# Kernel tuning notes

Hardware: AMD Instinct MI355X
Metric: run time of the kernel (lower is better)

## Reference

```python
import jax, jax.numpy as jnp
import numpy as np

T, B, E, H = 512, 64, 256, 256


def setup_inputs() -> dict:
    key = jax.random.key(0)
    ks = jax.random.split(key, 9)
    x = jax.random.normal(ks[0], (T * B, E), dtype=jnp.float32)
    # packed-sequence time reversal for equal-length sequences
    t = jnp.arange(T * B, dtype=jnp.int32)
    ix_mapping = (T - 1 - t // B) * B + (t % B)
    s = 0.05
    fw_W0 = jax.random.normal(ks[1], (3, E + H, H), dtype=jnp.float32) * s
    fw_W1 = jax.random.normal(ks[2], (3, 2 * H + H, H), dtype=jnp.float32) * s
    bw_W0 = jax.random.normal(ks[3], (3, E + H, H), dtype=jnp.float32) * s
    bw_W1 = jax.random.normal(ks[4], (3, 2 * H + H, H), dtype=jnp.float32) * s
    fw_b0 = jnp.zeros((3, H), jnp.float32)
    fw_b1 = jnp.zeros((3, H), jnp.float32)
    bw_b0 = jnp.zeros((3, H), jnp.float32)
    bw_b1 = jnp.zeros((3, H), jnp.float32)
    return dict(x=x, ix_mapping=ix_mapping, fw_W0=fw_W0, fw_b0=fw_b0,
                fw_W1=fw_W1, fw_b1=fw_b1, bw_W0=bw_W0, bw_b0=bw_b0,
                bw_W1=bw_W1, bw_b1=bw_b1)


def _run_direction(X_packed, W, b):
    # X_packed: [T*B, Din]; W: [3, Din+H, H] (r, h, z gates); b: [3, H]
    Din = X_packed.shape[1]
    X = X_packed.reshape(T, B, Din)

    def step(h, x_t):
        xh = jnp.concatenate((x_t, h), axis=1)          # [B, Din+H]
        r = jax.nn.sigmoid(xh @ W[0] + b[0])
        z = jax.nn.sigmoid(xh @ W[2] + b[2])
        xhr = jnp.concatenate((x_t, r * h), axis=1)
        cand = jnp.tanh(xhr @ W[1] + b[1])
        h_new = z * h + (1.0 - z) * cand
        return h_new, h_new

    h0 = jnp.zeros((B, X_packed.shape[1] * 0 + W.shape[2]), X_packed.dtype)
    h_n, states = jax.lax.scan(step, h0, X)
    return states.reshape(T * B, -1), h_n


def reference(x, ix_mapping, fw_W0, fw_b0, fw_W1, fw_b1,
              bw_W0, bw_b0, bw_W1, bw_b1):
    fwd_in = x
    bwd_in = x[ix_mapping]
    fw_params = [(fw_W0, fw_b0), (fw_W1, fw_b1)]
    bw_params = [(bw_W0, bw_b0), (bw_W1, bw_b1)]
    n_layers = len(fw_params)
    fh, bh = [], []
    for layer in range(n_layers):
        fs, fhn = _run_direction(fwd_in, *fw_params[layer])
        bs, bhn = _run_direction(bwd_in, *bw_params[layer])
        fh.append(fhn)
        bh.append(bhn)
        if layer < n_layers - 1:
            fwd_in = jnp.concatenate((fs, bs[ix_mapping]), axis=1)
            bwd_in = jnp.concatenate((bs, fs[ix_mapping]), axis=1)
    # MergeMethod.CONCAT
    out = jnp.concatenate((fs, bs[ix_mapping]), axis=1)  # [T*B, 2H]
    return out, jnp.stack(fh), jnp.stack(bh)
```

## Files before the change

kernel.cpp:

```cpp
#include <hip/hip_runtime.h>
#include <hip/hip_bf16.h>

#define T_STEPS 512
#define BATCH 64
#define TB (T_STEPS * BATCH)

typedef short bf16x8 __attribute__((ext_vector_type(8)));
typedef float f32x4 __attribute__((ext_vector_type(4)));

union FragU { uint4 u; bf16x8 v; };

static __device__ __forceinline__ bf16x8 ld_frag(const uint4* p) {
  FragU f; f.u = *p; return f.v;
}

static __device__ __forceinline__ unsigned short f2bf(float f) {
  unsigned u = __float_as_uint(f);
  return (unsigned short)((u + 0x7FFFu + ((u >> 16) & 1u)) >> 16);
}

static __device__ __forceinline__ unsigned cvt_pk_bf16(float lo, float hi) {
  unsigned r;
  asm("v_cvt_pk_bf16_f32 %0, %1, %2" : "=v"(r) : "v"(lo), "v"(hi));
  return r;
}

static __device__ __forceinline__ int revrow(int r) {
  int t = r >> 6, b = r & 63;
  return ((T_STEPS - 1 - t) << 6) | b;
}

#define S_RZ  (-1.4426950408889634f)
#define S_C   (-2.8853900817779268f)

#define AWR(N, x) asm volatile("v_accvgpr_write_b32 a" #N ", %0" :: "v"(x) : "a" #N)
#define LOADF(F, A0, A1, A2, A3) do { \
    const int c_ = (F) >> 3, kt_ = (F) & 7; \
    const int nt_ = (c_ < 2) ? (w * 2 + c_) : (14 + w * 2 + c_); \
    uint4 t = whrzp[((size_t)nt_ * 8 + kt_) * 64 + lane]; \
    AWR(A0, t.x); AWR(A1, t.y); AWR(A2, t.z); AWR(A3, t.w); } while (0)

#define MFMA_A(acc, va, B0, B3) \
  asm volatile("v_mfma_f32_16x16x32_bf16 %0, %1, a[" #B0 ":" #B3 "], %0" \
               : "+v"(acc) : "v"(va))
#define MFMA_A1(acc, va, B0, B3) \
  asm volatile("s_nop 1\n\tv_mfma_f32_16x16x32_bf16 %0, %1, a[" #B0 ":" #B3 "], %0" \
               : "+v"(acc) : "v"(va))
#define MFMA_V(acc, va, vb) \
  asm volatile("v_mfma_f32_16x16x32_bf16 %0, %1, %2, %0" \
               : "+v"(acc) : "v"(va), "v"(vb))
#define MFMA_V1(acc, va, vb) \
  asm volatile("s_nop 1\n\tv_mfma_f32_16x16x32_bf16 %0, %1, %2, %0" \
               : "+v"(acc) : "v"(va), "v"(vb))
#define ACCFENCE2(a, b) asm volatile("s_nop 7\n\ts_nop 7" : "+v"(a), "+v"(b))
#define ACCFENCE4(a, b, c, d) \
  asm volatile("s_nop 7\n\ts_nop 7" : "+v"(a), "+v"(b), "+v"(c), "+v"(d))

#define ACLB \
  "a0","a1","a2","a3","a4","a5","a6","a7","a8","a9","a10","a11","a12","a13","a14","a15", \
  "a16","a17","a18","a19","a20","a21","a22","a23","a24","a25","a26","a27","a28","a29","a30","a31", \
  "a32","a33","a34","a35","a36","a37","a38","a39","a40","a41","a42","a43","a44","a45","a46","a47", \
  "a48","a49","a50","a51","a52","a53","a54","a55","a56","a57","a58","a59","a60","a61","a62","a63", \
  "a64","a65","a66","a67","a68","a69","a70","a71","a72","a73","a74","a75","a76","a77","a78","a79", \
  "a80","a81","a82","a83","a84","a85","a86","a87","a88","a89","a90","a91","a92","a93","a94","a95", \
  "a96","a97","a98","a99","a100","a101","a102","a103","a104","a105","a106","a107","a108","a109","a110","a111", \
  "a112","a113","a114","a115","a116","a117","a118","a119","a120","a121","a122","a123","a124","a125","a126","a127"

__global__ void pack_w_kernel(const float* __restrict__ W, int rows, int k_base,
                              int n_tiles, int k_tiles, int mode,
                              unsigned short* __restrict__ dst) {
  int gid = blockIdx.x * blockDim.x + threadIdx.x;
  int total = n_tiles * k_tiles * 64;
  if (gid >= total) return;
  int lane = gid & 63;
  int fi = gid >> 6;
  int kt = fi % k_tiles;
  int nt = fi / k_tiles;
  int n = nt * 16 + (lane & 15);
  int g, col; float s;
  if (mode == 0)      { g = n >> 8;            col = n & 255; s = (g == 1) ? S_C : S_RZ; }
  else if (mode == 1) { g = (n < 256) ? 0 : 2; col = n & 255; s = S_RZ; }
  else                { g = 1;                 col = n;       s = S_C; }
  int k0 = k_base + kt * 32 + ((lane >> 4) << 3);
  const float* src = W + ((size_t)g * rows + k0) * 256 + col;
  unsigned short v[8];
#pragma unroll
  for (int j = 0; j < 8; ++j) v[j] = f2bf(src[(size_t)j * 256] * s);
  uint4 o;
  o.x = v[0] | ((unsigned)v[1] << 16);
  o.y = v[2] | ((unsigned)v[3] << 16);
  o.z = v[4] | ((unsigned)v[5] << 16);
  o.w = v[6] | ((unsigned)v[7] << 16);
  ((uint4*)dst)[gid] = o;
}

static __device__ __forceinline__ bf16x8 cvt8(float4 f0, float4 f1) {
  uint4 o;
  o.x = f2bf(f0.x) | ((unsigned)f2bf(f0.y) << 16);
  o.y = f2bf(f0.z) | ((unsigned)f2bf(f0.w) << 16);
  o.z = f2bf(f1.x) | ((unsigned)f2bf(f1.y) << 16);
  o.w = f2bf(f1.z) | ((unsigned)f2bf(f1.w) << 16);
  FragU f; f.u = o; return f.v;
}

template<int LAYER>
__global__ __launch_bounds__(256)
void gemm_xg_kernel(const float* __restrict__ x,
                    const unsigned short* __restrict__ fs0,
                    const unsigned short* __restrict__ bs0,
                    const unsigned short* __restrict__ Bp,
                    const float* __restrict__ bias_fw,
                    const float* __restrict__ bias_bw,
                    f32x4* __restrict__ Xg, int t0, int chunkT)
{
  constexpr int KT = (LAYER == 0) ? 8 : 16;
  int dir = blockIdx.z;
  int lane = threadIdx.x & 63;
  int w = threadIdx.x >> 6;
  int ww = w >> 1, wc = w & 1;
  int mt0 = blockIdx.x * 8 + ww * 4;
  int nt0 = blockIdx.y * 8 + wc * 4;
  const uint4* B = (const uint4*)Bp + (size_t)dir * 48 * KT * 64;
  const int arow = lane & 15;
  const int k0b = ((lane >> 4) << 3);

  f32x4 acc[4][4] = {};
#pragma unroll
  for (int kt = 0; kt < KT; ++kt) {
    int k0 = kt * 32 + k0b;
    bf16x8 a[4], b[4];
#pragma unroll
    for (int i = 0; i < 4; ++i) {
      int grow = t0 * 64 + (mt0 + i) * 16 + arow;
      if (LAYER == 0) {
        int gr = dir ? revrow(grow) : grow;
        const float4* s = (const float4*)(x + (size_t)gr * 256 + k0);
        a[i] = cvt8(s[0], s[1]);
      } else {
        const unsigned short* base; int r2 = grow, kk = k0;
        if (k0 < 256) { base = dir ? bs0 : fs0; }
        else          { base = dir ? fs0 : bs0; r2 = revrow(grow); kk = k0 - 256; }
        a[i] = *(const bf16x8*)(base + (size_t)r2 * 256 + kk);
      }
    }
#pragma unroll
    for (int j = 0; j < 4; ++j) b[j] = ld_frag(B + ((size_t)(nt0 + j) * KT + kt) * 64 + lane);
#pragma unroll
    for (int i = 0; i < 4; ++i)
#pragma unroll
      for (int j = 0; j < 4; ++j)
        acc[i][j] = __builtin_amdgcn_mfma_f32_16x16x32_bf16(a[i], b[j], acc[i][j], 0, 0, 0);
  }

  const float* bias = dir ? bias_bw : bias_fw;
  f32x4* C = Xg + (size_t)dir * (chunkT * 4) * 48 * 64;
#pragma unroll
  for (int j = 0; j < 4; ++j) {
    int ct = nt0 + j;
    int col = ct * 16 + (lane & 15);
    int g = col >> 8, cc = col & 255;
    float bv = ((g == 1) ? S_C : S_RZ) * bias[g * 256 + cc];
#pragma unroll
    for (int i = 0; i < 4; ++i) {
      int rt = blockIdx.x * 8 + ww * 4 + i;
      f32x4 v = acc[i][j];
      v[0] += bv; v[1] += bv; v[2] += bv; v[3] += bv;
      C[((size_t)rt * 48 + ct) * 64 + lane] = v;
    }
  }
}

template<int LAYER>
__global__ __launch_bounds__(512) __attribute__((amdgpu_waves_per_eu(2, 2)))
void gru_kernel(const f32x4* __restrict__ Xg,
                const uint4* __restrict__ whrz_fw, const uint4* __restrict__ whrz_bw,
                const uint4* __restrict__ whc_fw,  const uint4* __restrict__ whc_bw,
                unsigned short* __restrict__ sfw_bf, unsigned short* __restrict__ sbw_bf,
                float* __restrict__ out,
                float* __restrict__ hstate, float* __restrict__ dout_h,
                int t0, int chunkT)
{
  const int dir = blockIdx.y;
  const int bx = blockIdx.x;
  const int row0 = bx * 16;
  const int tid = threadIdx.x;
  const int lane = tid & 63;
  const int w = tid >> 6;

  __shared__ __align__(16) unsigned short h_bf[16 * 256];
  __shared__ __align__(16) unsigned short rh_bf[16 * 256];
  __shared__ __align__(16) uint4 wc_lds[16 * 8 * 64];

  const uint4* whrzp = dir ? whrz_bw : whrz_fw;
  const uint4* whcp  = dir ? whc_bw  : whc_fw;

  for (int i = tid; i < 16 * 8 * 64; i += 512) wc_lds[i] = whcp[i];

  LOADF(0, 0, 1, 2, 3);     LOADF(1, 4, 5, 6, 7);     LOADF(2, 8, 9, 10, 11);   LOADF(3, 12, 13, 14, 15);
  LOADF(4, 16, 17, 18, 19); LOADF(5, 20, 21, 22, 23); LOADF(6, 24, 25, 26, 27); LOADF(7, 28, 29, 30, 31);
  LOADF(8, 32, 33, 34, 35); LOADF(9, 36, 37, 38, 39); LOADF(10, 40, 41, 42, 43); LOADF(11, 44, 45, 46, 47);
  LOADF(12, 48, 49, 50, 51); LOADF(13, 52, 53, 54, 55); LOADF(14, 56, 57, 58, 59); LOADF(15, 60, 61, 62, 63);
  LOADF(16, 64, 65, 66, 67); LOADF(17, 68, 69, 70, 71); LOADF(18, 72, 73, 74, 75); LOADF(19, 76, 77, 78, 79);
  LOADF(20, 80, 81, 82, 83); LOADF(21, 84, 85, 86, 87); LOADF(22, 88, 89, 90, 91); LOADF(23, 92, 93, 94, 95);
  LOADF(24, 96, 97, 98, 99); LOADF(25, 100, 101, 102, 103); LOADF(26, 104, 105, 106, 107); LOADF(27, 108, 109, 110, 111);
  LOADF(28, 112, 113, 114, 115); LOADF(29, 116, 117, 118, 119); LOADF(30, 120, 121, 122, 123); LOADF(31, 124, 125, 126, 127);

  const int ccol = lane & 15;
  const int crow = ((lane >> 4) << 2);

  float* hst = hstate + (size_t)(dir * 4 + bx) * 4096;
  for (int i = tid; i < 16 * 256; i += 512) {
    float v = (t0 == 0) ? 0.0f : hst[i];
    int rr = i >> 8, cc = i & 255;
    int cb = cc * 2;
    int byt = rr * 512 + (((cb & ~15) ^ ((rr & 7) << 4)) | (cb & 15));
    *(unsigned short*)((char*)h_bf + byt) = f2bf(v);
  }
  float hreg[2][4];
#pragma unroll
  for (int j = 0; j < 2; ++j)
#pragma unroll
    for (int r = 0; r < 4; ++r) {
      int rr = crow + r, c = (w * 2 + j) * 16 + ccol;
      hreg[j][r] = (t0 == 0) ? 0.0f : hst[rr * 256 + c];
    }
  __syncthreads();

  const int ctR0 = w * 2, ctR1 = w * 2 + 1;
  const int ctZ0 = 32 + w * 2, ctZ1 = 33 + w * 2;
  const int ctB0c = 16 + w * 2, ctB1c = 17 + w * 2;
  const f32x4* XgD = Xg + (size_t)dir * (chunkT * 4) * 48 * 64;
  unsigned short* sp_bf = dir ? sbw_bf : sfw_bf;
  const int coff = dir ? 256 : 0;
  const int ardbase = (lane & 15) * 512;
  const int arxor = ((lane & 7) << 4);
  const int afc = ((lane >> 4) << 4);

#define AFRAG(KT) (*(const bf16x8*)((const char*)h_bf + (ardbase + ((KT * 64 + afc) ^ arxor))))
#define RFRAG(KT) (*(const bf16x8*)((const char*)rh_bf + (ardbase + ((KT * 64 + afc) ^ arxor))))
#define SWZ(rr, cb) ((rr) * 512 + ((((cb) & ~15) ^ (((rr) & 7) << 4)) | ((cb) & 15)))

  f32x4 xa0, xa1, xa2, xa3, xb0, xb1;
  {
    size_t rtb0 = ((size_t)(0 * 4 + bx) * 48) * 64 + lane;
    xa0 = XgD[rtb0 + (size_t)ctR0 * 64];
    xa1 = XgD[rtb0 + (size_t)ctR1 * 64];
    xa2 = XgD[rtb0 + (size_t)ctZ0 * 64];
    xa3 = XgD[rtb0 + (size_t)ctZ1 * 64];
    xb0 = XgD[rtb0 + (size_t)ctB0c * 64];
    xb1 = XgD[rtb0 + (size_t)ctB1c * 64];
  }

#pragma unroll 1
  for (int t = t0; t < t0 + chunkT; ++t) {
    const int tloc = t - t0;

    f32x4 accA0 = {}, accA1 = {}, accA2 = {}, accA3 = {};
    {
      bf16x8 af;
      af = AFRAG(0);
      MFMA_A1(accA0, af, 0, 3);   MFMA_A1(accA1, af, 32, 35);
      MFMA_A1(accA2, af, 64, 67); MFMA_A1(accA3, af, 96, 99);
      af = AFRAG(1);
      MFMA_A(accA0, af, 4, 7);    MFMA_A(accA1, af, 36, 39);
      MFMA_A(accA2, af, 68, 71);  MFMA_A(accA3, af, 100, 103);
      af = AFRAG(2);
      MFMA_A(accA0, af, 8, 11);   MFMA_A(accA1, af, 40, 43);
      MFMA_A(accA2, af, 72, 75);  MFMA_A(accA3, af, 104, 107);
      af = AFRAG(3);
      MFMA_A(accA0, af, 12, 15);  MFMA_A(accA1, af, 44, 47);
      MFMA_A(accA2, af, 76, 79);  MFMA_A(accA3, af, 108, 111);
      af = AFRAG(4);
      MFMA_A(accA0, af, 16, 19);  MFMA_A(accA1, af, 48, 51);
      MFMA_A(accA2, af, 80, 83);  MFMA_A(accA3, af, 112, 115);
      af = AFRAG(5);
      MFMA_A(accA0, af, 20, 23);  MFMA_A(accA1, af, 52, 55);
      MFMA_A(accA2, af, 84, 87);  MFMA_A(accA3, af, 116, 119);
      af = AFRAG(6);
      MFMA_A(accA0, af, 24, 27);  MFMA_A(accA1, af, 56, 59);
      MFMA_A(accA2, af, 88, 91);  MFMA_A(accA3, af, 120, 123);
      af = AFRAG(7);
      MFMA_A(accA0, af, 28, 31);  MFMA_A(accA1, af, 60, 63);
      MFMA_A(accA2, af, 92, 95);  MFMA_A(accA3, af, 124, 127);
    }
    ACCFENCE2(accA0, accA1);

#pragma unroll
    for (int j = 0; j < 2; ++j) {
      f32x4 ac = j ? accA1 : accA0;
      f32x4 xv = j ? xa1 : xa0;
      int cb = ((w * 2 + j) * 16 + ccol) * 2;
      float rh[4];
#pragma unroll
      for (int r = 0; r < 4; ++r) {
        float v = ac[r] + xv[r];
        float gate = __builtin_amdgcn_rcpf(1.0f + __builtin_amdgcn_exp2f(v));
        rh[r] = gate * hreg[j][r];
      }
      unsigned p01 = cvt_pk_bf16(rh[0], rh[1]);
      unsigned p23 = cvt_pk_bf16(rh[2], rh[3]);
      *(unsigned short*)((char*)rh_bf + SWZ(crow + 0, cb)) = (unsigned short)p01;
      *(unsigned short*)((char*)rh_bf + SWZ(crow + 1, cb)) = (unsigned short)(p01 >> 16);
      *(unsigned short*)((char*)rh_bf + SWZ(crow + 2, cb)) = (unsigned short)p23;
      *(unsigned short*)((char*)rh_bf + SWZ(crow + 3, cb)) = (unsigned short)(p23 >> 16);
    }
    asm volatile("s_waitcnt lgkmcnt(0)" ::: "memory", ACLB);
    __builtin_amdgcn_s_barrier();

    ACCFENCE2(accA2, accA3);
    float zreg[2][4];
#pragma unroll
    for (int j = 0; j < 2; ++j) {
      f32x4 ac = j ? accA3 : accA2;
      f32x4 xv = j ? xa3 : xa2;
#pragma unroll
      for (int r = 0; r < 4; ++r) {
        float v = ac[r] + xv[r];
        zreg[j][r] = __builtin_amdgcn_rcpf(1.0f + __builtin_amdgcn_exp2f(v));
      }
    }

    f32x4 accB0a = {}, accB0b = {}, accB1a = {}, accB1b = {};
#pragma unroll
    for (int kt = 0; kt < 4; ++kt) {
      bf16x8 a = RFRAG(kt);
      bf16x8 b0 = *(const bf16x8*)&wc_lds[((size_t)(w * 2 + 0) * 8 + kt) * 64 + lane];
      bf16x8 b1 = *(const bf16x8*)&wc_lds[((size_t)(w * 2 + 1) * 8 + kt) * 64 + lane];
      if (kt == 0) { MFMA_V1(accB0a, a, b0); MFMA_V1(accB1a, a, b1); }
      else         { MFMA_V(accB0a, a, b0);  MFMA_V(accB1a, a, b1); }
    }
#pragma unroll
    for (int kt = 4; kt < 8; ++kt) {
      bf16x8 a = RFRAG(kt);
      bf16x8 b0 = *(const bf16x8*)&wc_lds[((size_t)(w * 2 + 0) * 8 + kt) * 64 + lane];
      bf16x8 b1 = *(const bf16x8*)&wc_lds[((size_t)(w * 2 + 1) * 8 + kt) * 64 + lane];
      if (kt == 4) { MFMA_V1(accB0b, a, b0); MFMA_V1(accB1b, a, b1); }
      else         { MFMA_V(accB0b, a, b0);  MFMA_V(accB1b, a, b1); }
    }
    f32x4 cb0 = xb0, cb1 = xb1;
    {
      int tn = (tloc + 1 < chunkT) ? tloc + 1 : tloc;
      size_t rtn = ((size_t)(tn * 4 + bx) * 48) * 64 + lane;
      xa0 = XgD[rtn + (size_t)ctR0 * 64];
      xa1 = XgD[rtn + (size_t)ctR1 * 64];
      xa2 = XgD[rtn + (size_t)ctZ0 * 64];
      xa3 = XgD[rtn + (size_t)ctZ1 * 64];
      xb0 = XgD[rtn + (size_t)ctB0c * 64];
      xb1 = XgD[rtn + (size_t)ctB1c * 64];
    }
    ACCFENCE4(accB0a, accB0b, accB1a, accB1b);
    f32x4 accB0 = accB0a + accB0b;
    f32x4 accB1 = accB1a + accB1b;

    int gbase = (LAYER == 1 && dir) ? ((T_STEPS - 1 - t) * 64 + row0) : (t * 64 + row0);
#pragma unroll
    for (int j = 0; j < 2; ++j) {
      f32x4 ac = j ? accB1 : accB0;
      f32x4 xv = j ? cb1 : cb0;
      int c2 = (w * 2 + j) * 16 + ccol;
      int cb = c2 * 2;
      float hn[4];
#pragma unroll
      for (int r = 0; r < 4; ++r) {
        float v = ac[r] + xv[r];
        float cand = __builtin_amdgcn_rcpf(1.0f + __builtin_amdgcn_exp2f(v)) * 2.0f - 1.0f;
        hn[r] = cand + zreg[j][r] * (hreg[j][r] - cand);
        hreg[j][r] = hn[r];
      }
      unsigned p01 = cvt_pk_bf16(hn[0], hn[1]);
      unsigned p23 = cvt_pk_bf16(hn[2], hn[3]);
      *(unsigned short*)((char*)h_bf + SWZ(crow + 0, cb)) = (unsigned short)p01;
      *(unsigned short*)((char*)h_bf + SWZ(crow + 1, cb)) = (unsigned short)(p01 >> 16);
      *(unsigned short*)((char*)h_bf + SWZ(crow + 2, cb)) = (unsigned short)p23;
      *(unsigned short*)((char*)h_bf + SWZ(crow + 3, cb)) = (unsigned short)(p23 >> 16);
      if (LAYER == 0) {
        sp_bf[(size_t)(gbase + crow + 0) * 256 + c2] = (unsigned short)p01;
        sp_bf[(size_t)(gbase + crow + 1) * 256 + c2] = (unsigned short)(p01 >> 16);
        sp_bf[(size_t)(gbase + crow + 2) * 256 + c2] = (unsigned short)p23;
        sp_bf[(size_t)(gbase + crow + 3) * 256 + c2] = (unsigned short)(p23 >> 16);
      } else {
#pragma unroll
        for (int r = 0; r < 4; ++r)
          out[(size_t)(gbase + crow + r) * 512 + coff + c2] = hn[r];
      }
    }
    asm volatile("s_waitcnt lgkmcnt(0)" ::: "memory", ACLB);
    __builtin_amdgcn_s_barrier();
  }

#pragma unroll
  for (int j = 0; j < 2; ++j)
#pragma unroll
    for (int r = 0; r < 4; ++r) {
      int rr = crow + r, c = (w * 2 + j) * 16 + ccol;
      hst[rr * 256 + c] = hreg[j][r];
      if (t0 + chunkT == T_STEPS) {
        float* dst = dout_h + (dir ? 32768 : 0) + (size_t)LAYER * 16384;
        dst[(size_t)(row0 + rr) * 256 + c] = hreg[j][r];
      }
    }
}

__global__ void diag_kernel(float* out, float v) { out[0] = v; }

extern "C" void kernel_launch(void* const* d_in, const int* in_sizes, int n_in,
                              void* d_out, int out_size, void* d_ws, size_t ws_size,
                              hipStream_t stream) {
  const float* x     = (const float*)d_in[0];
  const float* fw_W0 = (const float*)d_in[2];
  const float* fw_b0 = (const float*)d_in[3];
  const float* fw_W1 = (const float*)d_in[4];
  const float* fw_b1 = (const float*)d_in[5];
  const float* bw_W0 = (const float*)d_in[6];
  const float* bw_b0 = (const float*)d_in[7];
  const float* bw_W1 = (const float*)d_in[8];
  const float* bw_b1 = (const float*)d_in[9];

  char* ws = (char*)d_ws;
  size_t off = 0;
  auto alloc = [&](size_t bytes) -> char* {
    char* p = ws + off; off += (bytes + 255) & ~(size_t)255; return p;
  };
  unsigned short* Wx0p  = (unsigned short*)alloc(2ull * 48 * 8 * 64 * 8 * 2);
  unsigned short* Wx1p  = (unsigned short*)alloc(2ull * 48 * 16 * 64 * 8 * 2);
  unsigned short* Whrz0 = (unsigned short*)alloc(2ull * 32 * 8 * 64 * 8 * 2);
  unsigned short* Whc0  = (unsigned short*)alloc(2ull * 16 * 8 * 64 * 8 * 2);
  unsigned short* Whrz1 = (unsigned short*)alloc(2ull * 32 * 8 * 64 * 8 * 2);
  unsigned short* Whc1  = (unsigned short*)alloc(2ull * 16 * 8 * 64 * 8 * 2);
  unsigned short* fs0   = (unsigned short*)alloc((size_t)TB * 256 * 2);
  unsigned short* bs0   = (unsigned short*)alloc((size_t)TB * 256 * 2);
  float* hstate         = (float*)alloc(2ull * 4 * 16 * 256 * 4);

  int chunkT = 0;
  for (int ct = 128; ct >= 8; ct >>= 1) {
    if (off + (size_t)ct * 2 * 64 * 768 * 4 <= ws_size) { chunkT = ct; break; }
  }
  float* out = (float*)d_out;
  if (chunkT == 0) {
    diag_kernel<<<1, 1, 0, stream>>>(out, 12345.0f);
    return;
  }
  f32x4* Xg = (f32x4*)alloc((size_t)chunkT * 2 * 64 * 768 * 4);
  float* dout_h = out + (size_t)TB * 512;

  auto packw = [&](const float* W, int rows, int kb, int ntl, int ktl, int mode, unsigned short* dst) {
    int total = ntl * ktl * 64;
    pack_w_kernel<<<(total + 255) / 256, 256, 0, stream>>>(W, rows, kb, ntl, ktl, mode, dst);
  };
  packw(fw_W0, 512, 0,   48, 8,  0, Wx0p);
  packw(bw_W0, 512, 0,   48, 8,  0, Wx0p + 48 * 8 * 64 * 8);
  packw(fw_W1, 768, 0,   48, 16, 0, Wx1p);
  packw(bw_W1, 768, 0,   48, 16, 0, Wx1p + 48 * 16 * 64 * 8);
  packw(fw_W0, 512, 256, 32, 8,  1, Whrz0);
  packw(bw_W0, 512, 256, 32, 8,  1, Whrz0 + 32 * 8 * 64 * 8);
  packw(fw_W0, 512, 256, 16, 8,  2, Whc0);
  packw(bw_W0, 512, 256, 16, 8,  2, Whc0 + 16 * 8 * 64 * 8);
  packw(fw_W1, 768, 512, 32, 8,  1, Whrz1);
  packw(bw_W1, 768, 512, 32, 8,  1, Whrz1 + 32 * 8 * 64 * 8);
  packw(fw_W1, 768, 512, 16, 8,  2, Whc1);
  packw(bw_W1, 768, 512, 16, 8,  2, Whc1 + 16 * 8 * 64 * 8);

  dim3 rgrid(4, 2);
  for (int t0 = 0; t0 < T_STEPS; t0 += chunkT) {
    dim3 ggrid(chunkT / 2, 6, 2);
    gemm_xg_kernel<0><<<ggrid, 256, 0, stream>>>(x, nullptr, nullptr, Wx0p, fw_b0, bw_b0, Xg, t0, chunkT);
    gru_kernel<0><<<rgrid, 512, 0, stream>>>(Xg,
        (const uint4*)Whrz0, (const uint4*)(Whrz0 + 32 * 8 * 64 * 8),
        (const uint4*)Whc0,  (const uint4*)(Whc0 + 16 * 8 * 64 * 8),
        fs0, bs0, nullptr, hstate, dout_h, t0, chunkT);
  }
  for (int t0 = 0; t0 < T_STEPS; t0 += chunkT) {
    dim3 ggrid(chunkT / 2, 6, 2);
    gemm_xg_kernel<1><<<ggrid, 256, 0, stream>>>(nullptr, fs0, bs0, Wx1p, fw_b1, bw_b1, Xg, t0, chunkT);
    gru_kernel<1><<<rgrid, 512, 0, stream>>>(Xg,
        (const uint4*)Whrz1, (const uint4*)(Whrz1 + 32 * 8 * 64 * 8),
        (const uint4*)Whc1,  (const uint4*)(Whc1 + 16 * 8 * 64 * 8),
        nullptr, nullptr, out, hstate, dout_h, t0, chunkT);
  }
}
```

Measured before the change: 2.550 ms.

## Use zero-operand MFMA init, precomputed LDS addresses, and larger time chunks

The first MFMA of each accumulator chain now reads a zero register as its C operand. This removes the accumulator zeroing and the s_nop padding before the chain. LDS read and write offsets plus global pointers for Xg, states and output are precomputed and advanced by stride each step, replacing per-step index arithmetic. The chunk size search now starts at 512, with padding so the last step's prefetch stays in bounds, which can mean fewer chunked launches if the workspace allows. This trims per-step instruction overhead in a serial recurrence loop, but adds register pressure from the held addresses.

```diff
diff --git a/kernel.cpp b/kernel.cpp
--- a/kernel.cpp
+++ b/kernel.cpp
@@ -43,15 +43,15 @@
 #define MFMA_A(acc, va, B0, B3) \
   asm volatile("v_mfma_f32_16x16x32_bf16 %0, %1, a[" #B0 ":" #B3 "], %0" \
                : "+v"(acc) : "v"(va))
-#define MFMA_A1(acc, va, B0, B3) \
-  asm volatile("s_nop 1\n\tv_mfma_f32_16x16x32_bf16 %0, %1, a[" #B0 ":" #B3 "], %0" \
-               : "+v"(acc) : "v"(va))
+#define MFMA_AZ(acc, va, B0, B3, zq) \
+  asm volatile("v_mfma_f32_16x16x32_bf16 %0, %1, a[" #B0 ":" #B3 "], %2" \
+               : "=&v"(acc) : "v"(va), "v"(zq))
 #define MFMA_V(acc, va, vb) \
   asm volatile("v_mfma_f32_16x16x32_bf16 %0, %1, %2, %0" \
                : "+v"(acc) : "v"(va), "v"(vb))
-#define MFMA_V1(acc, va, vb) \
-  asm volatile("s_nop 1\n\tv_mfma_f32_16x16x32_bf16 %0, %1, %2, %0" \
-               : "+v"(acc) : "v"(va), "v"(vb))
+#define MFMA_VZ(acc, va, vb, zq) \
+  asm volatile("v_mfma_f32_16x16x32_bf16 %0, %1, %2, %3" \
+               : "=&v"(acc) : "v"(va), "v"(vb), "v"(zq))
 #define ACCFENCE2(a, b) asm volatile("s_nop 7\n\ts_nop 7" : "+v"(a), "+v"(b))
 #define ACCFENCE4(a, b, c, d) \
   asm volatile("s_nop 7\n\ts_nop 7" : "+v"(a), "+v"(b), "+v"(c), "+v"(d))
@@ -187,8 +187,7 @@
   const int lane = tid & 63;
   const int w = tid >> 6;
 
-  __shared__ __align__(16) unsigned short h_bf[16 * 256];
-  __shared__ __align__(16) unsigned short rh_bf[16 * 256];
+  __shared__ __align__(16) unsigned short hx[2 * 16 * 256];
   __shared__ __align__(16) uint4 wc_lds[16 * 8 * 64];
 
   const uint4* whrzp = dir ? whrz_bw : whrz_fw;
@@ -208,13 +207,13 @@
   const int ccol = lane & 15;
   const int crow = ((lane >> 4) << 2);
 
+#define SWZ(rr, cb) ((rr) * 512 + ((((cb) & ~15) ^ (((rr) & 7) << 4)) | ((cb) & 15)))
+
   float* hst = hstate + (size_t)(dir * 4 + bx) * 4096;
   for (int i = tid; i < 16 * 256; i += 512) {
     float v = (t0 == 0) ? 0.0f : hst[i];
     int rr = i >> 8, cc = i & 255;
-    int cb = cc * 2;
-    int byt = rr * 512 + (((cb & ~15) ^ ((rr & 7) << 4)) | (cb & 15));
-    *(unsigned short*)((char*)h_bf + byt) = f2bf(v);
+    *(unsigned short*)((char*)hx + 8192 + SWZ(rr, cc * 2)) = f2bf(v);
   }
   float hreg[2][4];
 #pragma unroll
@@ -226,9 +225,6 @@
     }
   __syncthreads();
 
-  const int ctR0 = w * 2, ctR1 = w * 2 + 1;
-  const int ctZ0 = 32 + w * 2, ctZ1 = 33 + w * 2;
-  const int ctB0c = 16 + w * 2, ctB1c = 17 + w * 2;
   const f32x4* XgD = Xg + (size_t)dir * (chunkT * 4) * 48 * 64;
   unsigned short* sp_bf = dir ? sbw_bf : sfw_bf;
   const int coff = dir ? 256 : 0;
@@ -236,73 +232,92 @@
   const int arxor = ((lane & 7) << 4);
   const int afc = ((lane >> 4) << 4);
 
-#define AFRAG(KT) (*(const bf16x8*)((const char*)h_bf + (ardbase + ((KT * 64 + afc) ^ arxor))))
-#define RFRAG(KT) (*(const bf16x8*)((const char*)rh_bf + (ardbase + ((KT * 64 + afc) ^ arxor))))
-#define SWZ(rr, cb) ((rr) * 512 + ((((cb) & ~15) ^ (((rr) & 7) << 4)) | ((cb) & 15)))
-
-  f32x4 xa0, xa1, xa2, xa3, xb0, xb1;
-  {
-    size_t rtb0 = ((size_t)(0 * 4 + bx) * 48) * 64 + lane;
-    xa0 = XgD[rtb0 + (size_t)ctR0 * 64];
-    xa1 = XgD[rtb0 + (size_t)ctR1 * 64];
-    xa2 = XgD[rtb0 + (size_t)ctZ0 * 64];
-    xa3 = XgD[rtb0 + (size_t)ctZ1 * 64];
-    xb0 = XgD[rtb0 + (size_t)ctB0c * 64];
-    xb1 = XgD[rtb0 + (size_t)ctB1c * 64];
-  }
+  const int ra0 = ardbase + ((0 * 64 + afc) ^ arxor);
+  const int ra1 = ardbase + ((1 * 64 + afc) ^ arxor);
+  const int ra2 = ardbase + ((2 * 64 + afc) ^ arxor);
+  const int ra3 = ardbase + ((3 * 64 + afc) ^ arxor);
+  const int ra4 = ardbase + ((4 * 64 + afc) ^ arxor);
+  const int ra5 = ardbase + ((5 * 64 + afc) ^ arxor);
+  const int ra6 = ardbase + ((6 * 64 + afc) ^ arxor);
+  const int ra7 = ardbase + ((7 * 64 + afc) ^ arxor);
+#define HF(RA)  (*(const bf16x8*)((const char*)hx + 8192 + (RA)))
+#define RHF(RA) (*(const bf16x8*)((const char*)hx + (RA)))
+
+  const int cbj0 = ((w * 2 + 0) * 16 + ccol) * 2;
+  const int cbj1 = ((w * 2 + 1) * 16 + ccol) * 2;
+  const int wa00 = SWZ(crow + 0, cbj0), wa01 = SWZ(crow + 1, cbj0);
+  const int wa02 = SWZ(crow + 2, cbj0), wa03 = SWZ(crow + 3, cbj0);
+  const int wa10 = SWZ(crow + 0, cbj1), wa11 = SWZ(crow + 1, cbj1);
+  const int wa12 = SWZ(crow + 2, cbj1), wa13 = SWZ(crow + 3, cbj1);
+
+  const size_t XSTEP = (size_t)4 * 48 * 64;
+  const f32x4* pR = XgD + (size_t)bx * 48 * 64 + (size_t)(w * 2) * 64 + lane;
+  const f32x4* pZ = pR + (size_t)32 * 64;
+  const f32x4* pB = pR + (size_t)16 * 64;
+
+  unsigned short* pSp = sp_bf + ((size_t)(t0 * 64 + row0 + crow) * 256) + (w * 2) * 16 + ccol;
+  const int g0 = (LAYER == 1 && dir) ? ((T_STEPS - 1 - t0) * 64 + row0) : (t0 * 64 + row0);
+  float* pO = out ? out + ((size_t)(g0 + crow) * 512) + coff + (w * 2) * 16 + ccol : nullptr;
+  float* pO2 = pO ? pO + 2 * 512 : nullptr;
+  const long long OSTEP = (LAYER == 1 && dir) ? -(long long)64 * 512 : (long long)64 * 512;
+
+  f32x4 zq = {0.0f, 0.0f, 0.0f, 0.0f};
+
+  f32x4 xa0 = pR[0], xa1 = pR[64], xa2 = pZ[0], xa3 = pZ[64], xb0 = pB[0], xb1 = pB[64];
 
 #pragma unroll 1
   for (int t = t0; t < t0 + chunkT; ++t) {
-    const int tloc = t - t0;
-
-    f32x4 accA0 = {}, accA1 = {}, accA2 = {}, accA3 = {};
+    f32x4 accA0, accA1, accA2, accA3;
     {
       bf16x8 af;
-      af = AFRAG(0);
-      MFMA_A1(accA0, af, 0, 3);   MFMA_A1(accA1, af, 32, 35);
-      MFMA_A1(accA2, af, 64, 67); MFMA_A1(accA3, af, 96, 99);
-      af = AFRAG(1);
+      af = HF(ra0);
+      MFMA_AZ(accA0, af, 0, 3, zq);   MFMA_AZ(accA1, af, 32, 35, zq);
+      MFMA_AZ(accA2, af, 64, 67, zq); MFMA_AZ(accA3, af, 96, 99, zq);
+      af = HF(ra1);
       MFMA_A(accA0, af, 4, 7);    MFMA_A(accA1, af, 36, 39);
       MFMA_A(accA2, af, 68, 71);  MFMA_A(accA3, af, 100, 103);
-      af = AFRAG(2);
+      af = HF(ra2);
       MFMA_A(accA0, af, 8, 11);   MFMA_A(accA1, af, 40, 43);
       MFMA_A(accA2, af, 72, 75);  MFMA_A(accA3, af, 104, 107);
-      af = AFRAG(3);
+      af = HF(ra3);
       MFMA_A(accA0, af, 12, 15);  MFMA_A(accA1, af, 44, 47);
       MFMA_A(accA2, af, 76, 79);  MFMA_A(accA3, af, 108, 111);
-      af = AFRAG(4);
+      af = HF(ra4);
       MFMA_A(accA0, af, 16, 19);  MFMA_A(accA1, af, 48, 51);
       MFMA_A(accA2, af, 80, 83);  MFMA_A(accA3, af, 112, 115);
-      af = AFRAG(5);
+      af = HF(ra5);
       MFMA_A(accA0, af, 20, 23);  MFMA_A(accA1, af, 52, 55);
       MFMA_A(accA2, af, 84, 87);  MFMA_A(accA3, af, 116, 119);
-      af = AFRAG(6);
+      af = HF(ra6);
       MFMA_A(accA0, af, 24, 27);  MFMA_A(accA1, af, 56, 59);
       MFMA_A(accA2, af, 88, 91);  MFMA_A(accA3, af, 120, 123);
-      af = AFRAG(7);
+      af = HF(ra7);
       MFMA_A(accA0, af, 28, 31);  MFMA_A(accA1, af, 60, 63);
       MFMA_A(accA2, af, 92, 95);  MFMA_A(accA3, af, 124, 127);
     }
     ACCFENCE2(accA0, accA1);
 
-#pragma unroll
-    for (int j = 0; j < 2; ++j) {
-      f32x4 ac = j ? accA1 : accA0;
-      f32x4 xv = j ? xa1 : xa0;
-      int cb = ((w * 2 + j) * 16 + ccol) * 2;
-      float rh[4];
+    {
+      float rh0[4], rh1[4];
 #pragma unroll
       for (int r = 0; r < 4; ++r) {
-        float v = ac[r] + xv[r];
-        float gate = __builtin_amdgcn_rcpf(1.0f + __builtin_amdgcn_exp2f(v));
-        rh[r] = gate * hreg[j][r];
+        float v0 = accA0[r] + xa0[r];
+        rh0[r] = __builtin_amdgcn_rcpf(1.0f + __builtin_amdgcn_exp2f(v0)) * hreg[0][r];
+        float v1 = accA1[r] + xa1[r];
+        rh1[r] = __builtin_amdgcn_rcpf(1.0f + __builtin_amdgcn_exp2f(v1)) * hreg[1][r];
       }
-      unsigned p01 = cvt_pk_bf16(rh[0], rh[1]);
-      unsigned p23 = cvt_pk_bf16(rh[2], rh[3]);
-      *(unsigned short*)((char*)rh_bf + SWZ(crow + 0, cb)) = (unsigned short)p01;
-      *(unsigned short*)((char*)rh_bf + SWZ(crow + 1, cb)) = (unsigned short)(p01 >> 16);
-      *(unsigned short*)((char*)rh_bf + SWZ(crow + 2, cb)) = (unsigned short)p23;
-      *(unsigned short*)((char*)rh_bf + SWZ(crow + 3, cb)) = (unsigned short)(p23 >> 16);
+      unsigned a01 = cvt_pk_bf16(rh0[0], rh0[1]);
+      unsigned a23 = cvt_pk_bf16(rh0[2], rh0[3]);
+      unsigned b01 = cvt_pk_bf16(rh1[0], rh1[1]);
+      unsigned b23 = cvt_pk_bf16(rh1[2], rh1[3]);
+      *(unsigned short*)((char*)hx + wa00) = (unsigned short)a01;
+      *(unsigned short*)((char*)hx + wa01) = (unsigned short)(a01 >> 16);
+      *(unsigned short*)((char*)hx + wa02) = (unsigned short)a23;
+      *(unsigned short*)((char*)hx + wa03) = (unsigned short)(a23 >> 16);
+      *(unsigned short*)((char*)hx + wa10) = (unsigned short)b01;
+      *(unsigned short*)((char*)hx + wa11) = (unsigned short)(b01 >> 16);
+      *(unsigned short*)((char*)hx + wa12) = (unsigned short)b23;
+      *(unsigned short*)((char*)hx + wa13) = (unsigned short)(b23 >> 16);
     }
     asm volatile("s_waitcnt lgkmcnt(0)" ::: "memory", ACLB);
     __builtin_amdgcn_s_barrier();
@@ -310,55 +325,51 @@
     ACCFENCE2(accA2, accA3);
     float zreg[2][4];
 #pragma unroll
-    for (int j = 0; j < 2; ++j) {
-      f32x4 ac = j ? accA3 : accA2;
-      f32x4 xv = j ? xa3 : xa2;
-#pragma unroll
-      for (int r = 0; r < 4; ++r) {
-        float v = ac[r] + xv[r];
-        zreg[j][r] = __builtin_amdgcn_rcpf(1.0f + __builtin_amdgcn_exp2f(v));
-      }
-    }
-
-    f32x4 accB0a = {}, accB0b = {}, accB1a = {}, accB1b = {};
-#pragma unroll
-    for (int kt = 0; kt < 4; ++kt) {
-      bf16x8 a = RFRAG(kt);
-      bf16x8 b0 = *(const bf16x8*)&wc_lds[((size_t)(w * 2 + 0) * 8 + kt) * 64 + lane];
-      bf16x8 b1 = *(const bf16x8*)&wc_lds[((size_t)(w * 2 + 1) * 8 + kt) * 64 + lane];
-      if (kt == 0) { MFMA_V1(accB0a, a, b0); MFMA_V1(accB1a, a, b1); }
-      else         { MFMA_V(accB0a, a, b0);  MFMA_V(accB1a, a, b1); }
-    }
-#pragma unroll
-    for (int kt = 4; kt < 8; ++kt) {
-      bf16x8 a = RFRAG(kt);
-      bf16x8 b0 = *(const bf16x8*)&wc_lds[((size_t)(w * 2 + 0) * 8 + kt) * 64 + lane];
-      bf16x8 b1 = *(const bf16x8*)&wc_lds[((size_t)(w * 2 + 1) * 8 + kt) * 64 + lane];
-      if (kt == 4) { MFMA_V1(accB0b, a, b0); MFMA_V1(accB1b, a, b1); }
-      else         { MFMA_V(accB0b, a, b0);  MFMA_V(accB1b, a, b1); }
+    for (int r = 0; r < 4; ++r) {
+      zreg[0][r] = __builtin_amdgcn_rcpf(1.0f + __builtin_amdgcn_exp2f(accA2[r] + xa2[r]));
+      zreg[1][r] = __builtin_amdgcn_rcpf(1.0f + __builtin_amdgcn_exp2f(accA3[r] + xa3[r]));
+    }
+
+    f32x4 accB0a, accB0b, accB1a, accB1b;
+    {
+      bf16x8 a;
+      a = RHF(ra0);
+      MFMA_VZ(accB0a, a, *(const bf16x8*)&wc_lds[((size_t)(w * 2 + 0) * 8 + 0) * 64 + lane], zq);
+      MFMA_VZ(accB1a, a, *(const bf16x8*)&wc_lds[((size_t)(w * 2 + 1) * 8 + 0) * 64 + lane], zq);
+      a = RHF(ra1);
+      MFMA_V(accB0a, a, *(const bf16x8*)&wc_lds[((size_t)(w * 2 + 0) * 8 + 1) * 64 + lane]);
+      MFMA_V(accB1a, a, *(const bf16x8*)&wc_lds[((size_t)(w * 2 + 1) * 8 + 1) * 64 + lane]);
+      a = RHF(ra2);
+      MFMA_V(accB0a, a, *(const bf16x8*)&wc_lds[((size_t)(w * 2 + 0) * 8 + 2) * 64 + lane]);
+      MFMA_V(accB1a, a, *(const bf16x8*)&wc_lds[((size_t)(w * 2 + 1) * 8 + 2) * 64 + lane]);
+      a = RHF(ra3);
+      MFMA_V(accB0a, a, *(const bf16x8*)&wc_lds[((size_t)(w * 2 + 0) * 8 + 3) * 64 + lane]);
+      MFMA_V(accB1a, a, *(const bf16x8*)&wc_lds[((size_t)(w * 2 + 1) * 8 + 3) * 64 + lane]);
+      a = RHF(ra4);
+      MFMA_VZ(accB0b, a, *(const bf16x8*)&wc_lds[((size_t)(w * 2 + 0) * 8 + 4) * 64 + lane], zq);
+      MFMA_VZ(accB1b, a, *(const bf16x8*)&wc_lds[((size_t)(w * 2 + 1) * 8 + 4) * 64 + lane], zq);
+      a = RHF(ra5);
+      MFMA_V(accB0b, a, *(const bf16x8*)&wc_lds[((size_t)(w * 2 + 0) * 8 + 5) * 64 + lane]);
+      MFMA_V(accB1b, a, *(const bf16x8*)&wc_lds[((size_t)(w * 2 + 1) * 8 + 5) * 64 + lane]);
+      a = RHF(ra6);
+      MFMA_V(accB0b, a, *(const bf16x8*)&wc_lds[((size_t)(w * 2 + 0) * 8 + 6) * 64 + lane]);
+      MFMA_V(accB1b, a, *(const bf16x8*)&wc_lds[((size_t)(w * 2 + 1) * 8 + 6) * 64 + lane]);
+      a = RHF(ra7);
+      MFMA_V(accB0b, a, *(const bf16x8*)&wc_lds[((size_t)(w * 2 + 0) * 8 + 7) * 64 + lane]);
+      MFMA_V(accB1b, a, *(const bf16x8*)&wc_lds[((size_t)(w * 2 + 1) * 8 + 7) * 64 + lane]);
     }
     f32x4 cb0 = xb0, cb1 = xb1;
-    {
-      int tn = (tloc + 1 < chunkT) ? tloc + 1 : tloc;
-      size_t rtn = ((size_t)(tn * 4 + bx) * 48) * 64 + lane;
-      xa0 = XgD[rtn + (size_t)ctR0 * 64];
-      xa1 = XgD[rtn + (size_t)ctR1 * 64];
-      xa2 = XgD[rtn + (size_t)ctZ0 * 64];
-      xa3 = XgD[rtn + (size_t)ctZ1 * 64];
-      xb0 = XgD[rtn + (size_t)ctB0c * 64];
-      xb1 = XgD[rtn + (size_t)ctB1c * 64];
-    }
+    pR += XSTEP; pZ += XSTEP; pB += XSTEP;
+    xa0 = pR[0]; xa1 = pR[64]; xa2 = pZ[0]; xa3 = pZ[64]; xb0 = pB[0]; xb1 = pB[64];
+
     ACCFENCE4(accB0a, accB0b, accB1a, accB1b);
     f32x4 accB0 = accB0a + accB0b;
     f32x4 accB1 = accB1a + accB1b;
 
-    int gbase = (LAYER == 1 && dir) ? ((T_STEPS - 1 - t) * 64 + row0) : (t * 64 + row0);
 #pragma unroll
     for (int j = 0; j < 2; ++j) {
       f32x4 ac = j ? accB1 : accB0;
       f32x4 xv = j ? cb1 : cb0;
-      int c2 = (w * 2 + j) * 16 + ccol;
-      int cb = c2 * 2;
       float hn[4];
 #pragma unroll
       for (int r = 0; r < 4; ++r) {
@@ -369,21 +380,27 @@
       }
       unsigned p01 = cvt_pk_bf16(hn[0], hn[1]);
       unsigned p23 = cvt_pk_bf16(hn[2], hn[3]);
-      *(unsigned short*)((char*)h_bf + SWZ(crow + 0, cb)) = (unsigned short)p01;
-      *(unsigned short*)((char*)h_bf + SWZ(crow + 1, cb)) = (unsigned short)(p01 >> 16);
-      *(unsigned short*)((char*)h_bf + SWZ(crow + 2, cb)) = (unsigned short)p23;
-      *(unsigned short*)((char*)h_bf + SWZ(crow + 3, cb)) = (unsigned short)(p23 >> 16);
+      int wA = j ? wa10 : wa00, wB = j ? wa11 : wa01;
+      int wC = j ? wa12 : wa02, wD = j ? wa13 : wa03;
+      *(unsigned short*)((char*)hx + 8192 + wA) = (unsigned short)p01;
+      *(unsigned short*)((char*)hx + 8192 + wB) = (unsigned short)(p01 >> 16);
+      *(unsigned short*)((char*)hx + 8192 + wC) = (unsigned short)p23;
+      *(unsigned short*)((char*)hx + 8192 + wD) = (unsigned short)(p23 >> 16);
       if (LAYER == 0) {
-        sp_bf[(size_t)(gbase + crow + 0) * 256 + c2] = (unsigned short)p01;
-        sp_bf[(size_t)(gbase + crow + 1) * 256 + c2] = (unsigned short)(p01 >> 16);
-        sp_bf[(size_t)(gbase + crow + 2) * 256 + c2] = (unsigned short)p23;
-        sp_bf[(size_t)(gbase + crow + 3) * 256 + c2] = (unsigned short)(p23 >> 16);
+        pSp[(size_t)j * 16 + 0 * 256] = (unsigned short)p01;
+        pSp[(size_t)j * 16 + 1 * 256] = (unsigned short)(p01 >> 16);
+        pSp[(size_t)j * 16 + 2 * 256] = (unsigned short)p23;
+        pSp[(size_t)j * 16 + 3 * 256] = (unsigned short)(p23 >> 16);
       } else {
-#pragma unroll
-        for (int r = 0; r < 4; ++r)
-          out[(size_t)(gbase + crow + r) * 512 + coff + c2] = hn[r];
+        pO[(size_t)j * 16 + 0 * 512] = hn[0];
+        pO[(size_t)j * 16 + 1 * 512] = hn[1];
+        pO2[(size_t)j * 16 + 0 * 512] = hn[2];
+        pO2[(size_t)j * 16 + 1 * 512] = hn[3];
       }
     }
+    if (LAYER == 0) pSp += (size_t)64 * 256;
+    else { pO += OSTEP; pO2 += OSTEP; }
+
     asm volatile("s_waitcnt lgkmcnt(0)" ::: "memory", ACLB);
     __builtin_amdgcn_s_barrier();
   }
@@ -431,16 +448,17 @@
   unsigned short* bs0   = (unsigned short*)alloc((size_t)TB * 256 * 2);
   float* hstate         = (float*)alloc(2ull * 4 * 16 * 256 * 4);
 
+  const size_t XPAD = (size_t)4 * 48 * 64 * 16;
   int chunkT = 0;
-  for (int ct = 128; ct >= 8; ct >>= 1) {
-    if (off + (size_t)ct * 2 * 64 * 768 * 4 <= ws_size) { chunkT = ct; break; }
+  for (int ct = 512; ct >= 8; ct >>= 1) {
+    if (off + (size_t)ct * 2 * 64 * 768 * 4 + XPAD <= ws_size) { chunkT = ct; break; }
   }
   float* out = (float*)d_out;
   if (chunkT == 0) {
     diag_kernel<<<1, 1, 0, stream>>>(out, 12345.0f);
     return;
   }
-  f32x4* Xg = (f32x4*)alloc((size_t)chunkT * 2 * 64 * 768 * 4);
+  f32x4* Xg = (f32x4*)alloc((size_t)chunkT * 2 * 64 * 768 * 4 + XPAD);
   float* dout_h = out + (size_t)TB * 512;
 
   auto packw = [&](const float* W, int rows, int kb, int ntl, int ktl, int mode, unsigned short* dst) {
```

New measurement: 2.505 ms. About the same (-1.8%).
